# Kernel tuning notes

Measured on AMD Instinct MI355X. Metric: run time of the kernel, lower is better.

Reference implementation:

```python
import jax, jax.numpy as jnp
import numpy as np

B, S, D, H = 2, 2048, 1024, 16
Dh = D // H
ROPE_BASE = 10000.0


def _rope_cos_sin(seq_len, dh, dtype):
    inv_freq = 1.0 / (ROPE_BASE ** (jnp.arange(0, dh, 2, dtype=jnp.float32) / dh))
    t = jnp.arange(seq_len, dtype=jnp.float32)
    freqs = jnp.outer(t, inv_freq)              # (S, Dh/2)
    emb = jnp.concatenate([freqs, freqs], -1)   # (S, Dh)
    return jnp.cos(emb).astype(dtype), jnp.sin(emb).astype(dtype)


def _rotate_half(x):
    x1, x2 = jnp.split(x, 2, axis=-1)
    return jnp.concatenate([-x2, x1], axis=-1)


def setup_inputs() -> dict:
    key = jax.random.key(0)
    k1, k2, k3 = jax.random.split(key, 3)
    x = jax.random.normal(k1, (B, S, D), dtype=jnp.float32)
    w_qkv = jax.random.normal(k2, (D, 3 * D), dtype=jnp.float32) * (1.0 / np.sqrt(D))
    w_proj = jax.random.normal(k3, (D, D), dtype=jnp.float32) * (1.0 / np.sqrt(D))
    return {"x": x, "w_qkv": w_qkv, "w_proj": w_proj}


def reference(x, w_qkv, w_proj):
    b, s, d = x.shape
    qkv = x @ w_qkv                              # (B, S, 3D)
    q, k, v = jnp.split(qkv, 3, axis=-1)
    # (B, S, D) -> (B, H, S, Dh)
    shape_heads = lambda t: t.reshape(b, s, H, Dh).transpose(0, 2, 1, 3)
    q, k, v = shape_heads(q), shape_heads(k), shape_heads(v)
    cos, sin = _rope_cos_sin(s, Dh, x.dtype)     # (S, Dh) each
    cos = cos[None, None]                        # (1,1,S,Dh)
    sin = sin[None, None]
    q = q * cos + _rotate_half(q) * sin
    k = k * cos + _rotate_half(k) * sin
    attn = jnp.einsum('bhqd,bhkd->bhqk', q, k) / np.sqrt(Dh).astype(x.dtype)
    causal_mask = jnp.tril(jnp.ones((s, s), dtype=bool))
    attn = jnp.where(causal_mask, attn, -jnp.inf)
    attn = jax.nn.softmax(attn, axis=-1)
    out = jnp.einsum('bhqk,bhkd->bhqd', attn, v)
    out = out.transpose(0, 2, 1, 3).reshape(b, s, d)
    return out @ w_proj
```

## Files before the change

### kernel.cpp

```cpp
#include <hip/hip_runtime.h>


typedef unsigned short u16;
typedef __bf16 bf16x8 __attribute__((ext_vector_type(8)));
typedef unsigned short u16x8 __attribute__((ext_vector_type(8)));
typedef unsigned short u16x4 __attribute__((ext_vector_type(4)));
typedef float f32x4 __attribute__((ext_vector_type(4)));

#define B_ 2
#define S_ 2048
#define D_ 1024
#define H_ 16
#define DH_ 64
#define BS_ (B_ * S_)
#define N3_ (3 * D_)

__device__ __forceinline__ u16 f2bf(float f) {
  unsigned u = __float_as_uint(f);
  u += 0x7FFFu + ((u >> 16) & 1u);
  return (u16)(u >> 16);
}
__device__ __forceinline__ float bf2f(u16 s) {
  return __uint_as_float(((unsigned)s) << 16);
}

union BU { u16x8 u; bf16x8 b; };

__device__ __forceinline__ void store_c(u16* C, size_t i, float v) { C[i] = f2bf(v); }
__device__ __forceinline__ void store_c(float* C, size_t i, float v) { C[i] = v; }

#define SWZ(r) ((((r) >> 1) & 3) << 4)

__global__ __launch_bounds__(256) void k_cvt(const float* __restrict__ in,
                                             u16* __restrict__ out, int n4) {
  int i = blockIdx.x * 256 + threadIdx.x;
  if (i >= n4) return;
  const float4 f = ((const float4*)in)[i];
  u16x4 o;
  o[0] = f2bf(f.x); o[1] = f2bf(f.y); o[2] = f2bf(f.z); o[3] = f2bf(f.w);
  *(u16x4*)(out + (size_t)i * 4) = o;
}

__global__ __launch_bounds__(256) void k_cvt_T(const float* __restrict__ w,
                                               u16* __restrict__ wT, int R, int C) {
  __shared__ float tl[32][33];
  const int t = threadIdx.x;
  const int lrow = t >> 3, seg = t & 7;
  const int r0 = blockIdx.y * 32, c0 = blockIdx.x * 32;
  const float4 f = *(const float4*)(w + (size_t)(r0 + lrow) * C + c0 + seg * 4);
  tl[lrow][seg * 4 + 0] = f.x; tl[lrow][seg * 4 + 1] = f.y;
  tl[lrow][seg * 4 + 2] = f.z; tl[lrow][seg * 4 + 3] = f.w;
  __syncthreads();
  u16x4 o;
#pragma unroll
  for (int j = 0; j < 4; ++j) o[j] = f2bf(tl[seg * 4 + j][lrow]);
  *(u16x4*)(wT + (size_t)(c0 + lrow) * R + r0 + seg * 4) = o;
}

__global__ __launch_bounds__(256) void k_tab(float* __restrict__ ct, float* __restrict__ st) {
  const int idx = blockIdx.x * 256 + threadIdx.x;
  const int tpos = idx >> 5, i = idx & 31;
  const float invf = powf(10000.0f, -(float)i * (1.0f / 32.0f));
  const float a = (float)tpos * invf;
  ct[idx] = cosf(a);
  st[idx] = sinf(a);
}

template <typename OutT>
__global__ __launch_bounds__(256) void k_gemm(const u16* __restrict__ A,
                                              const u16* __restrict__ BT,
                                              OutT* __restrict__ C,
                                              int M, int N, int K) {
  __shared__ u16 la[128 * 32];
  __shared__ u16 lb[128 * 32];
  const int t = threadIdx.x;
  const int m0 = blockIdx.y * 128, n0 = blockIdx.x * 128;
  const int w = t >> 6, lane = t & 63;
  const int lr = lane & 15, lg = lane >> 4;
  const int wm = (w >> 1) * 64, wn = (w & 1) * 64;
  const int NK = K >> 5;

  const int r0s = t >> 2, i0 = t & 3;
  const int r1s = r0s + 64;

  f32x4 acc[4][4] = {};

  const u16* Ab = A + (size_t)m0 * K;
  const u16* Bb = BT + (size_t)n0 * K;

  u16x8 sa0 = *(const u16x8*)(Ab + (size_t)r0s * K + i0 * 8);
  u16x8 sa1 = *(const u16x8*)(Ab + (size_t)r1s * K + i0 * 8);
  u16x8 sb0 = *(const u16x8*)(Bb + (size_t)r0s * K + i0 * 8);
  u16x8 sb1 = *(const u16x8*)(Bb + (size_t)r1s * K + i0 * 8);
  u16x8 na0 = sa0, na1 = sa1, nb0 = sb0, nb1 = sb1;

  char* laq = (char*)la;
  char* lbq = (char*)lb;
  const int wo0 = r0s * 64 + ((i0 * 16) ^ SWZ(r0s));
  const int wo1 = r1s * 64 + ((i0 * 16) ^ SWZ(r1s));

  for (int kt = 0; kt < NK; ++kt) {
    __syncthreads();
    *(u16x8*)(laq + wo0) = sa0;
    *(u16x8*)(laq + wo1) = sa1;
    *(u16x8*)(lbq + wo0) = sb0;
    *(u16x8*)(lbq + wo1) = sb1;
    __syncthreads();
    if (kt + 1 < NK) {
      const u16* Ak = Ab + (size_t)(kt + 1) * 32;
      const u16* Bk = Bb + (size_t)(kt + 1) * 32;
      na0 = *(const u16x8*)(Ak + (size_t)r0s * K + i0 * 8);
      na1 = *(const u16x8*)(Ak + (size_t)r1s * K + i0 * 8);
      nb0 = *(const u16x8*)(Bk + (size_t)r0s * K + i0 * 8);
      nb1 = *(const u16x8*)(Bk + (size_t)r1s * K + i0 * 8);
    }
    BU af[4], bf_[4];
#pragma unroll
    for (int mi = 0; mi < 4; ++mi) {
      const int row = wm + mi * 16 + lr;
      af[mi].u = *(const u16x8*)(laq + row * 64 + ((lg * 16) ^ SWZ(row)));
      const int rowb = wn + mi * 16 + lr;
      bf_[mi].u = *(const u16x8*)(lbq + rowb * 64 + ((lg * 16) ^ SWZ(rowb)));
    }
#pragma unroll
    for (int mi = 0; mi < 4; ++mi)
#pragma unroll
      for (int ni = 0; ni < 4; ++ni)
        acc[mi][ni] = __builtin_amdgcn_mfma_f32_16x16x32_bf16(af[mi].b, bf_[ni].b,
                                                              acc[mi][ni], 0, 0, 0);
    sa0 = na0; sa1 = na1; sb0 = nb0; sb1 = nb1;
  }

#pragma unroll
  for (int mi = 0; mi < 4; ++mi)
#pragma unroll
    for (int ni = 0; ni < 4; ++ni)
#pragma unroll
      for (int r = 0; r < 4; ++r) {
        const int row = m0 + wm + mi * 16 + lg * 4 + r;
        const int col = n0 + wn + ni * 16 + lr;
        store_c(C, (size_t)row * N + col, acc[mi][ni][r]);
      }
}

__global__ __launch_bounds__(256) void k_prep(const u16* __restrict__ qkv,
                                              const float* __restrict__ ct,
                                              const float* __restrict__ st,
                                              u16* __restrict__ Q, u16* __restrict__ K,
                                              u16* __restrict__ Vt) {
  __shared__ u16 vl[64][72];
  const int stile = blockIdx.x, bh = blockIdx.y;
  const int b = bh >> 4, h = bh & 15;
  const int t = threadIdx.x;
  const int row = t >> 2, qr = t & 3;
  const int s = stile * 64 + row;
  const u16* base = qkv + (size_t)(b * S_ + s) * N3_ + h * DH_;
  const int d0 = qr * 8;
  float c[8], sn[8];
#pragma unroll
  for (int j = 0; j < 8; ++j) {
    c[j] = ct[s * 32 + d0 + j];
    sn[j] = st[s * 32 + d0 + j];
  }
#pragma unroll
  for (int part = 0; part < 2; ++part) {
    const u16* src = base + part * D_;
    u16x8 lo = *(const u16x8*)(src + d0);
    u16x8 hi = *(const u16x8*)(src + d0 + 32);
    u16x8 olo, ohi;
#pragma unroll
    for (int j = 0; j < 8; ++j) {
      float x1 = bf2f(lo[j]), x2 = bf2f(hi[j]);
      olo[j] = f2bf(x1 * c[j] - x2 * sn[j]);
      ohi[j] = f2bf(x2 * c[j] + x1 * sn[j]);
    }
    u16* dst = (part ? K : Q) + ((size_t)bh * S_ + s) * DH_;
    *(u16x8*)(dst + d0) = olo;
    *(u16x8*)(dst + d0 + 32) = ohi;
  }
  u16x8 v0 = *(const u16x8*)(base + 2 * D_ + qr * 16);
  u16x8 v1 = *(const u16x8*)(base + 2 * D_ + qr * 16 + 8);
#pragma unroll
  for (int j = 0; j < 8; ++j) {
    vl[qr * 16 + j][row] = v0[j];
    vl[qr * 16 + 8 + j][row] = v1[j];
  }
  __syncthreads();
  const int dh = row, sc = qr * 16;
  u16x8 o0, o1;
#pragma unroll
  for (int j = 0; j < 8; ++j) { o0[j] = vl[dh][sc + j]; o1[j] = vl[dh][sc + 8 + j]; }
  u16* vdst = Vt + ((size_t)bh * DH_ + dh) * S_ + stile * 64 + sc;
  *(u16x8*)vdst = o0;
  *(u16x8*)(vdst + 8) = o1;
}

__global__ __launch_bounds__(256, 4) void k_attn(const u16* __restrict__ Q,
                                                 const u16* __restrict__ K,
                                                 const u16* __restrict__ Vt,
                                                 u16* __restrict__ Ao) {
  __shared__ char kvb_[2][16384];
  __shared__ char plb[4][2048];
  const int bid = blockIdx.x;
  const int xcd = bid & 7, inner = bid >> 3;
  const int bh = xcd + 8 * (inner & 3);
  const int qt = 31 - (inner >> 2);
  const int t = threadIdx.x;
  const int w = t >> 6, lane = t & 63;
  const int lr = lane & 15, lg = lane >> 4;
  const int q0 = qt * 64 + w * 16;
  const int nt = qt + 1;

  const u16* Kbh = K + (size_t)bh * S_ * DH_;
  const u16* Vbh = Vt + (size_t)bh * DH_ * S_;

  const int srow = t >> 3;
  const int scol = (t & 7) * 8;

  const u16* Qb = Q + ((size_t)bh * S_ + q0) * DH_;
  BU qf0, qf1;
  qf0.u = *(const u16x8*)(Qb + lr * DH_ + lg * 8);
  qf1.u = *(const u16x8*)(Qb + lr * DH_ + 32 + lg * 8);

  f32x4 o[4] = {};
  float m = -1e30f, l = 0.f;
  char* plw = plb[w];
  const int psw = (lr & 7) << 4;

  u16x8 kreg[2], vreg[2];
#pragma unroll
  for (int c = 0; c < 2; ++c) {
    const int row = srow + 32 * c;
    kreg[c] = *(const u16x8*)(Kbh + (size_t)row * DH_ + scol);
    vreg[c] = *(const u16x8*)(Vbh + (size_t)row * S_ + scol);
  }
  {
    char* dst = kvb_[0];
#pragma unroll
    for (int c = 0; c < 2; ++c) {
      const int row = srow + 32 * c;
      const int off = row * 128 + ((scol * 2) ^ ((row & 7) << 4));
      *(u16x8*)(dst + off) = kreg[c];
      *(u16x8*)(dst + 8192 + off) = vreg[c];
    }
  }
  __syncthreads();

  int cur = 0;
  for (int it = 0; it < nt; ++it) {
    const int kv0 = it * 64;
    if (it + 1 < nt) {
      const int kvn = kv0 + 64;
#pragma unroll
      for (int c = 0; c < 2; ++c) {
        const int row = srow + 32 * c;
        kreg[c] = *(const u16x8*)(Kbh + (size_t)(kvn + row) * DH_ + scol);
        vreg[c] = *(const u16x8*)(Vbh + (size_t)row * S_ + kvn + scol);
      }
    }
    const char* base = kvb_[cur];
    f32x4 s[4] = {};
#pragma unroll
    for (int kvbi = 0; kvbi < 4; ++kvbi) {
      const int row = kvbi * 16 + lr;
      const int sw = (lr & 7) << 4;
      BU k0, k1;
      k0.u = *(const u16x8*)(base + row * 128 + ((lg * 16) ^ sw));
      k1.u = *(const u16x8*)(base + row * 128 + ((64 + lg * 16) ^ sw));
      s[kvbi] = __builtin_amdgcn_mfma_f32_16x16x32_bf16(k0.b, qf0.b, s[kvbi], 0, 0, 0);
      s[kvbi] = __builtin_amdgcn_mfma_f32_16x16x32_bf16(k1.b, qf1.b, s[kvbi], 0, 0, 0);
    }
    float p[16];
#pragma unroll
    for (int kvbi = 0; kvbi < 4; ++kvbi)
#pragma unroll
      for (int r = 0; r < 4; ++r) p[kvbi * 4 + r] = s[kvbi][r] * 0.125f;
    if (it == nt - 1) {
#pragma unroll
      for (int kvbi = 0; kvbi < 4; ++kvbi)
#pragma unroll
        for (int r = 0; r < 4; ++r)
          if (kv0 + kvbi * 16 + lg * 4 + r > q0 + lr) p[kvbi * 4 + r] = -1e30f;
    }
    float mx = p[0];
#pragma unroll
    for (int i = 1; i < 16; ++i) mx = fmaxf(mx, p[i]);
    mx = fmaxf(mx, __shfl_xor(mx, 16, 64));
    mx = fmaxf(mx, __shfl_xor(mx, 32, 64));
    const float mn = fmaxf(m, mx);
    const float al = __expf(m - mn);
    m = mn;
    float sm = 0.f;
#pragma unroll
    for (int i = 0; i < 16; ++i) { p[i] = __expf(p[i] - mn); sm += p[i]; }
    sm += __shfl_xor(sm, 16, 64);
    sm += __shfl_xor(sm, 32, 64);
    l = l * al + sm;
#pragma unroll
    for (int d = 0; d < 4; ++d)
#pragma unroll
      for (int r = 0; r < 4; ++r) o[d][r] *= al;
#pragma unroll
    for (int kvbi = 0; kvbi < 4; ++kvbi) {
      u16x4 w4;
#pragma unroll
      for (int r = 0; r < 4; ++r) w4[r] = f2bf(p[kvbi * 4 + r]);
      *(u16x4*)(plw + lr * 128 + ((kvbi * 32 + lg * 8) ^ psw)) = w4;
    }
    BU pf0, pf1;
    pf0.u = *(const u16x8*)(plw + lr * 128 + ((lg * 16) ^ psw));
    pf1.u = *(const u16x8*)(plw + lr * 128 + ((64 + lg * 16) ^ psw));
#pragma unroll
    for (int d = 0; d < 4; ++d) {
      const int row = d * 16 + lr;
      const int sw = (lr & 7) << 4;
      BU v0, v1;
      v0.u = *(const u16x8*)(base + 8192 + row * 128 + ((lg * 16) ^ sw));
      v1.u = *(const u16x8*)(base + 8192 + row * 128 + ((64 + lg * 16) ^ sw));
      o[d] = __builtin_amdgcn_mfma_f32_16x16x32_bf16(v0.b, pf0.b, o[d], 0, 0, 0);
      o[d] = __builtin_amdgcn_mfma_f32_16x16x32_bf16(v1.b, pf1.b, o[d], 0, 0, 0);
    }
    if (it + 1 < nt) {
      char* dst = kvb_[cur ^ 1];
#pragma unroll
      for (int c = 0; c < 2; ++c) {
        const int row = srow + 32 * c;
        const int off = row * 128 + ((scol * 2) ^ ((row & 7) << 4));
        *(u16x8*)(dst + off) = kreg[c];
        *(u16x8*)(dst + 8192 + off) = vreg[c];
      }
      __syncthreads();
    }
    cur ^= 1;
  }

  const float inv = 1.0f / l;
  const int b = bh >> 4, h = bh & 15;
  const size_t rowo = ((size_t)b * S_ + q0 + lr) * D_ + h * DH_;
#pragma unroll
  for (int d = 0; d < 4; ++d) {
    u16x4 w4;
#pragma unroll
    for (int r = 0; r < 4; ++r) w4[r] = f2bf(o[d][r] * inv);
    *(u16x4*)(Ao + rowo + d * 16 + lg * 4) = w4;
  }
}

extern "C" void kernel_launch(void* const* d_in, const int* in_sizes, int n_in,
                              void* d_out, int out_size, void* d_ws, size_t ws_size,
                              hipStream_t stream) {
  const float* x = (const float*)d_in[0];
  const float* wqkv = (const float*)d_in[1];
  const float* wproj = (const float*)d_in[2];
  float* out = (float*)d_out;
  char* ws = (char*)d_ws;

  u16* xb      = (u16*)(ws + 0);
  u16* wqkvT   = (u16*)(ws + 8388608);
  u16* wprojT  = (u16*)(ws + 14680064);
  u16* qkvb    = (u16*)(ws + 16777216);
  u16* Qb      = (u16*)(ws + 41943040);
  u16* Kb      = (u16*)(ws + 50331648);
  u16* Vtb     = (u16*)(ws + 58720256);
  u16* aob     = (u16*)(ws + 67108864);
  float* ct    = (float*)(ws + 75497472);
  float* stab  = (float*)(ws + 75759616);

  k_cvt<<<4096, 256, 0, stream>>>(x, xb, BS_ * D_ / 4);
  k_cvt_T<<<dim3(96, 32), 256, 0, stream>>>(wqkv, wqkvT, D_, N3_);
  k_cvt_T<<<dim3(32, 32), 256, 0, stream>>>(wproj, wprojT, D_, D_);
  k_tab<<<256, 256, 0, stream>>>(ct, stab);

  k_gemm<u16><<<dim3(24, 32), 256, 0, stream>>>(xb, wqkvT, qkvb, BS_, N3_, D_);
  k_prep<<<dim3(32, 32), 256, 0, stream>>>(qkvb, ct, stab, Qb, Kb, Vtb);
  k_attn<<<1024, 256, 0, stream>>>(Qb, Kb, Vtb, aob);
  k_gemm<float><<<dim3(8, 32), 256, 0, stream>>>(aob, wprojT, out, BS_, D_, D_);
}
```

Measured before the change: 126.5 us.

## Use direct global-to-LDS loads, pair causal q-tiles, fold softmax scale into Q

The GEMM now stages A/B tiles with global_load_lds into double-buffered LDS, dropping the register round trip and one barrier per k-step. Attention does the same for K/V, and each block handles a short and a long causal q-tile pair, halving the grid to balance work. The 1/sqrt(Dh) scale moves into the Q RoPE prep, and the softmax rescale is skipped unless the running max grows by more than 8. The launch bound drops to 2 blocks per CU. Risks: lower occupancy, the lazy-rescale threshold loosens overflow margins, and the LDS swizzle layout must match the reads exactly.

```diff
diff --git a/kernel.cpp b/kernel.cpp
--- a/kernel.cpp
+++ b/kernel.cpp
@@ -2,6 +2,7 @@
 
 
 typedef unsigned short u16;
+typedef unsigned int u32;
 typedef __bf16 bf16x8 __attribute__((ext_vector_type(8)));
 typedef unsigned short u16x8 __attribute__((ext_vector_type(8)));
 typedef unsigned short u16x4 __attribute__((ext_vector_type(4)));
@@ -29,7 +30,11 @@
 __device__ __forceinline__ void store_c(u16* C, size_t i, float v) { C[i] = f2bf(v); }
 __device__ __forceinline__ void store_c(float* C, size_t i, float v) { C[i] = v; }
 
-#define SWZ(r) ((((r) >> 1) & 3) << 4)
+__device__ __forceinline__ void gl16(const void* g, void* l) {
+  __builtin_amdgcn_global_load_lds(
+      (const __attribute__((address_space(1))) u32*)g,
+      (__attribute__((address_space(3))) u32*)l, 16, 0, 0);
+}
 
 __global__ __launch_bounds__(256) void k_cvt(const float* __restrict__ in,
                                              u16* __restrict__ out, int n4) {
@@ -71,8 +76,8 @@
                                               const u16* __restrict__ BT,
                                               OutT* __restrict__ C,
                                               int M, int N, int K) {
-  __shared__ u16 la[128 * 32];
-  __shared__ u16 lb[128 * 32];
+  __shared__ u16 la[2][128 * 32];
+  __shared__ u16 lb[2][128 * 32];
   const int t = threadIdx.x;
   const int m0 = blockIdx.y * 128, n0 = blockIdx.x * 128;
   const int w = t >> 6, lane = t & 63;
@@ -80,55 +85,50 @@
   const int wm = (w >> 1) * 64, wn = (w & 1) * 64;
   const int NK = K >> 5;
 
-  const int r0s = t >> 2, i0 = t & 3;
-  const int r1s = r0s + 64;
+  const int srow = lane >> 2;
+  const int sc = ((lane & 3) ^ ((lane >> 3) & 3)) * 8;
+  const u16* Ag = A + (size_t)(m0 + w * 32 + srow) * K + sc;
+  const u16* Bg = BT + (size_t)(n0 + w * 32 + srow) * K + sc;
+  const int ldsw = w * 1024;
 
   f32x4 acc[4][4] = {};
 
-  const u16* Ab = A + (size_t)m0 * K;
-  const u16* Bb = BT + (size_t)n0 * K;
-
-  u16x8 sa0 = *(const u16x8*)(Ab + (size_t)r0s * K + i0 * 8);
-  u16x8 sa1 = *(const u16x8*)(Ab + (size_t)r1s * K + i0 * 8);
-  u16x8 sb0 = *(const u16x8*)(Bb + (size_t)r0s * K + i0 * 8);
-  u16x8 sb1 = *(const u16x8*)(Bb + (size_t)r1s * K + i0 * 8);
-  u16x8 na0 = sa0, na1 = sa1, nb0 = sb0, nb1 = sb1;
-
-  char* laq = (char*)la;
-  char* lbq = (char*)lb;
-  const int wo0 = r0s * 64 + ((i0 * 16) ^ SWZ(r0s));
-  const int wo1 = r1s * 64 + ((i0 * 16) ^ SWZ(r1s));
-
+#pragma unroll
+  for (int i = 0; i < 2; ++i) {
+    gl16(Ag + (size_t)i * 16 * K, la[0] + ldsw + i * 512);
+    gl16(Bg + (size_t)i * 16 * K, lb[0] + ldsw + i * 512);
+  }
+  __syncthreads();
+
+  int cur = 0;
   for (int kt = 0; kt < NK; ++kt) {
+    if (kt + 1 < NK) {
+      const int ko = (kt + 1) * 32;
+#pragma unroll
+      for (int i = 0; i < 2; ++i) {
+        gl16(Ag + (size_t)i * 16 * K + ko, la[cur ^ 1] + ldsw + i * 512);
+        gl16(Bg + (size_t)i * 16 * K + ko, lb[cur ^ 1] + ldsw + i * 512);
+      }
+    }
+    const char* pa = (const char*)la[cur];
+    const char* pb = (const char*)lb[cur];
+    BU af[4], bfr[4];
+    const int rsw = ((lr >> 1) & 3);
+#pragma unroll
+    for (int mi = 0; mi < 4; ++mi) {
+      const int ra = wm + mi * 16 + lr;
+      af[mi].u = *(const u16x8*)(pa + ra * 64 + ((lg ^ rsw) * 16));
+      const int rb = wn + mi * 16 + lr;
+      bfr[mi].u = *(const u16x8*)(pb + rb * 64 + ((lg ^ rsw) * 16));
+    }
+#pragma unroll
+    for (int mi = 0; mi < 4; ++mi)
+#pragma unroll
+      for (int ni = 0; ni < 4; ++ni)
+        acc[mi][ni] = __builtin_amdgcn_mfma_f32_16x16x32_bf16(af[mi].b, bfr[ni].b,
+                                                              acc[mi][ni], 0, 0, 0);
     __syncthreads();
-    *(u16x8*)(laq + wo0) = sa0;
-    *(u16x8*)(laq + wo1) = sa1;
-    *(u16x8*)(lbq + wo0) = sb0;
-    *(u16x8*)(lbq + wo1) = sb1;
-    __syncthreads();
-    if (kt + 1 < NK) {
-      const u16* Ak = Ab + (size_t)(kt + 1) * 32;
-      const u16* Bk = Bb + (size_t)(kt + 1) * 32;
-      na0 = *(const u16x8*)(Ak + (size_t)r0s * K + i0 * 8);
-      na1 = *(const u16x8*)(Ak + (size_t)r1s * K + i0 * 8);
-      nb0 = *(const u16x8*)(Bk + (size_t)r0s * K + i0 * 8);
-      nb1 = *(const u16x8*)(Bk + (size_t)r1s * K + i0 * 8);
-    }
-    BU af[4], bf_[4];
-#pragma unroll
-    for (int mi = 0; mi < 4; ++mi) {
-      const int row = wm + mi * 16 + lr;
-      af[mi].u = *(const u16x8*)(laq + row * 64 + ((lg * 16) ^ SWZ(row)));
-      const int rowb = wn + mi * 16 + lr;
-      bf_[mi].u = *(const u16x8*)(lbq + rowb * 64 + ((lg * 16) ^ SWZ(rowb)));
-    }
-#pragma unroll
-    for (int mi = 0; mi < 4; ++mi)
-#pragma unroll
-      for (int ni = 0; ni < 4; ++ni)
-        acc[mi][ni] = __builtin_amdgcn_mfma_f32_16x16x32_bf16(af[mi].b, bf_[ni].b,
-                                                              acc[mi][ni], 0, 0, 0);
-    sa0 = na0; sa1 = na1; sb0 = nb0; sb1 = nb1;
+    cur ^= 1;
   }
 
 #pragma unroll
@@ -164,13 +164,14 @@
   }
 #pragma unroll
   for (int part = 0; part < 2; ++part) {
+    const float qs = (part == 0) ? 0.125f : 1.0f;
     const u16* src = base + part * D_;
     u16x8 lo = *(const u16x8*)(src + d0);
     u16x8 hi = *(const u16x8*)(src + d0 + 32);
     u16x8 olo, ohi;
 #pragma unroll
     for (int j = 0; j < 8; ++j) {
-      float x1 = bf2f(lo[j]), x2 = bf2f(hi[j]);
+      float x1 = bf2f(lo[j]) * qs, x2 = bf2f(hi[j]) * qs;
       olo[j] = f2bf(x1 * c[j] - x2 * sn[j]);
       ohi[j] = f2bf(x2 * c[j] + x1 * sn[j]);
     }
@@ -195,7 +196,7 @@
   *(u16x8*)(vdst + 8) = o1;
 }
 
-__global__ __launch_bounds__(256, 4) void k_attn(const u16* __restrict__ Q,
+__global__ __launch_bounds__(256, 2) void k_attn(const u16* __restrict__ Q,
                                                  const u16* __restrict__ K,
                                                  const u16* __restrict__ Vt,
                                                  u16* __restrict__ Ao) {
@@ -204,145 +205,135 @@
   const int bid = blockIdx.x;
   const int xcd = bid & 7, inner = bid >> 3;
   const int bh = xcd + 8 * (inner & 3);
-  const int qt = 31 - (inner >> 2);
+  const int f = inner >> 2;
   const int t = threadIdx.x;
   const int w = t >> 6, lane = t & 63;
   const int lr = lane & 15, lg = lane >> 4;
-  const int q0 = qt * 64 + w * 16;
-  const int nt = qt + 1;
 
   const u16* Kbh = K + (size_t)bh * S_ * DH_;
   const u16* Vbh = Vt + (size_t)bh * DH_ * S_;
 
-  const int srow = t >> 3;
-  const int scol = (t & 7) * 8;
-
-  const u16* Qb = Q + ((size_t)bh * S_ + q0) * DH_;
-  BU qf0, qf1;
-  qf0.u = *(const u16x8*)(Qb + lr * DH_ + lg * 8);
-  qf1.u = *(const u16x8*)(Qb + lr * DH_ + 32 + lg * 8);
-
-  f32x4 o[4] = {};
-  float m = -1e30f, l = 0.f;
+  const int sr = lane >> 3;
+  const int sc = ((lane & 7) ^ sr) * 8;
+  char* kd0 = kvb_[0] + w * 2048;
+  char* kd1 = kvb_[1] + w * 2048;
+
   char* plw = plb[w];
   const int psw = (lr & 7) << 4;
-
-  u16x8 kreg[2], vreg[2];
-#pragma unroll
-  for (int c = 0; c < 2; ++c) {
-    const int row = srow + 32 * c;
-    kreg[c] = *(const u16x8*)(Kbh + (size_t)row * DH_ + scol);
-    vreg[c] = *(const u16x8*)(Vbh + (size_t)row * S_ + scol);
-  }
-  {
-    char* dst = kvb_[0];
-#pragma unroll
-    for (int c = 0; c < 2; ++c) {
-      const int row = srow + 32 * c;
-      const int off = row * 128 + ((scol * 2) ^ ((row & 7) << 4));
-      *(u16x8*)(dst + off) = kreg[c];
-      *(u16x8*)(dst + 8192 + off) = vreg[c];
-    }
-  }
-  __syncthreads();
-
-  int cur = 0;
-  for (int it = 0; it < nt; ++it) {
-    const int kv0 = it * 64;
-    if (it + 1 < nt) {
-      const int kvn = kv0 + 64;
-#pragma unroll
-      for (int c = 0; c < 2; ++c) {
-        const int row = srow + 32 * c;
-        kreg[c] = *(const u16x8*)(Kbh + (size_t)(kvn + row) * DH_ + scol);
-        vreg[c] = *(const u16x8*)(Vbh + (size_t)row * S_ + kvn + scol);
-      }
-    }
-    const char* base = kvb_[cur];
-    f32x4 s[4] = {};
-#pragma unroll
-    for (int kvbi = 0; kvbi < 4; ++kvbi) {
-      const int row = kvbi * 16 + lr;
-      const int sw = (lr & 7) << 4;
-      BU k0, k1;
-      k0.u = *(const u16x8*)(base + row * 128 + ((lg * 16) ^ sw));
-      k1.u = *(const u16x8*)(base + row * 128 + ((64 + lg * 16) ^ sw));
-      s[kvbi] = __builtin_amdgcn_mfma_f32_16x16x32_bf16(k0.b, qf0.b, s[kvbi], 0, 0, 0);
-      s[kvbi] = __builtin_amdgcn_mfma_f32_16x16x32_bf16(k1.b, qf1.b, s[kvbi], 0, 0, 0);
-    }
-    float p[16];
-#pragma unroll
-    for (int kvbi = 0; kvbi < 4; ++kvbi)
-#pragma unroll
-      for (int r = 0; r < 4; ++r) p[kvbi * 4 + r] = s[kvbi][r] * 0.125f;
-    if (it == nt - 1) {
+  const int b = bh >> 4, h = bh & 15;
+
+  for (int ph = 0; ph < 2; ++ph) {
+    const int qt = ph ? 31 - f : f;
+    const int q0 = qt * 64 + w * 16;
+    const int nt = qt + 1;
+
+    const u16* Qb = Q + ((size_t)bh * S_ + q0) * DH_;
+    BU qf0, qf1;
+    qf0.u = *(const u16x8*)(Qb + lr * DH_ + lg * 8);
+    qf1.u = *(const u16x8*)(Qb + lr * DH_ + 32 + lg * 8);
+
+    f32x4 o[4] = {};
+    float m = -1e30f, l = 0.f;
+
+    __syncthreads();
+#pragma unroll
+    for (int j = 0; j < 2; ++j) {
+      const int row = w * 16 + j * 8 + sr;
+      gl16(Kbh + (size_t)row * DH_ + sc, kd0 + j * 1024);
+      gl16(Vbh + (size_t)row * S_ + sc, kd0 + 8192 + j * 1024);
+    }
+    __syncthreads();
+
+    int cur = 0;
+    for (int it = 0; it < nt; ++it) {
+      const int kv0 = it * 64;
+      if (it + 1 < nt) {
+        const int kvn = kv0 + 64;
+        char* nd = cur ? kd0 : kd1;
+#pragma unroll
+        for (int j = 0; j < 2; ++j) {
+          const int row = w * 16 + j * 8 + sr;
+          gl16(Kbh + (size_t)(kvn + row) * DH_ + sc, nd + j * 1024);
+          gl16(Vbh + (size_t)row * S_ + kvn + sc, nd + 8192 + j * 1024);
+        }
+      }
+      const char* base = kvb_[cur];
+      f32x4 s[4] = {};
+#pragma unroll
+      for (int kvbi = 0; kvbi < 4; ++kvbi) {
+        const int row = kvbi * 16 + lr;
+        const int sw = (lr & 7) << 4;
+        BU k0, k1;
+        k0.u = *(const u16x8*)(base + row * 128 + ((lg * 16) ^ sw));
+        k1.u = *(const u16x8*)(base + row * 128 + ((64 + lg * 16) ^ sw));
+        s[kvbi] = __builtin_amdgcn_mfma_f32_16x16x32_bf16(k0.b, qf0.b, s[kvbi], 0, 0, 0);
+        s[kvbi] = __builtin_amdgcn_mfma_f32_16x16x32_bf16(k1.b, qf1.b, s[kvbi], 0, 0, 0);
+      }
+      float p[16];
 #pragma unroll
       for (int kvbi = 0; kvbi < 4; ++kvbi)
 #pragma unroll
-        for (int r = 0; r < 4; ++r)
-          if (kv0 + kvbi * 16 + lg * 4 + r > q0 + lr) p[kvbi * 4 + r] = -1e30f;
-    }
-    float mx = p[0];
-#pragma unroll
-    for (int i = 1; i < 16; ++i) mx = fmaxf(mx, p[i]);
-    mx = fmaxf(mx, __shfl_xor(mx, 16, 64));
-    mx = fmaxf(mx, __shfl_xor(mx, 32, 64));
-    const float mn = fmaxf(m, mx);
-    const float al = __expf(m - mn);
-    m = mn;
-    float sm = 0.f;
-#pragma unroll
-    for (int i = 0; i < 16; ++i) { p[i] = __expf(p[i] - mn); sm += p[i]; }
-    sm += __shfl_xor(sm, 16, 64);
-    sm += __shfl_xor(sm, 32, 64);
-    l = l * al + sm;
-#pragma unroll
-    for (int d = 0; d < 4; ++d)
-#pragma unroll
-      for (int r = 0; r < 4; ++r) o[d][r] *= al;
-#pragma unroll
-    for (int kvbi = 0; kvbi < 4; ++kvbi) {
+        for (int r = 0; r < 4; ++r) p[kvbi * 4 + r] = s[kvbi][r];
+      if (it == nt - 1) {
+#pragma unroll
+        for (int kvbi = 0; kvbi < 4; ++kvbi)
+#pragma unroll
+          for (int r = 0; r < 4; ++r)
+            if (kv0 + kvbi * 16 + lg * 4 + r > q0 + lr) p[kvbi * 4 + r] = -1e30f;
+      }
+      float mx = p[0];
+#pragma unroll
+      for (int i = 1; i < 16; ++i) mx = fmaxf(mx, p[i]);
+      mx = fmaxf(mx, __shfl_xor(mx, 16, 64));
+      mx = fmaxf(mx, __shfl_xor(mx, 32, 64));
+      float al = 1.f;
+      const bool resc = (mx > m + 8.f);
+      if (resc) { al = __expf(m - mx); m = mx; }
+      float sm = 0.f;
+#pragma unroll
+      for (int i = 0; i < 16; ++i) { p[i] = __expf(p[i] - m); sm += p[i]; }
+      sm += __shfl_xor(sm, 16, 64);
+      sm += __shfl_xor(sm, 32, 64);
+      l = l * al + sm;
+      if (resc) {
+#pragma unroll
+        for (int d = 0; d < 4; ++d)
+#pragma unroll
+          for (int r = 0; r < 4; ++r) o[d][r] *= al;
+      }
+#pragma unroll
+      for (int kvbi = 0; kvbi < 4; ++kvbi) {
+        u16x4 w4;
+#pragma unroll
+        for (int r = 0; r < 4; ++r) w4[r] = f2bf(p[kvbi * 4 + r]);
+        *(u16x4*)(plw + lr * 128 + ((kvbi * 32 + lg * 8) ^ psw)) = w4;
+      }
+      BU pf0, pf1;
+      pf0.u = *(const u16x8*)(plw + lr * 128 + ((lg * 16) ^ psw));
+      pf1.u = *(const u16x8*)(plw + lr * 128 + ((64 + lg * 16) ^ psw));
+#pragma unroll
+      for (int d = 0; d < 4; ++d) {
+        const int row = d * 16 + lr;
+        const int sw = (lr & 7) << 4;
+        BU v0, v1;
+        v0.u = *(const u16x8*)(base + 8192 + row * 128 + ((lg * 16) ^ sw));
+        v1.u = *(const u16x8*)(base + 8192 + row * 128 + ((64 + lg * 16) ^ sw));
+        o[d] = __builtin_amdgcn_mfma_f32_16x16x32_bf16(v0.b, pf0.b, o[d], 0, 0, 0);
+        o[d] = __builtin_amdgcn_mfma_f32_16x16x32_bf16(v1.b, pf1.b, o[d], 0, 0, 0);
+      }
+      __syncthreads();
+      cur ^= 1;
+    }
+
+    const float inv = 1.0f / l;
+    const size_t rowo = ((size_t)b * S_ + q0 + lr) * D_ + h * DH_;
+#pragma unroll
+    for (int d = 0; d < 4; ++d) {
       u16x4 w4;
 #pragma unroll
-      for (int r = 0; r < 4; ++r) w4[r] = f2bf(p[kvbi * 4 + r]);
-      *(u16x4*)(plw + lr * 128 + ((kvbi * 32 + lg * 8) ^ psw)) = w4;
-    }
-    BU pf0, pf1;
-    pf0.u = *(const u16x8*)(plw + lr * 128 + ((lg * 16) ^ psw));
-    pf1.u = *(const u16x8*)(plw + lr * 128 + ((64 + lg * 16) ^ psw));
-#pragma unroll
-    for (int d = 0; d < 4; ++d) {
-      const int row = d * 16 + lr;
-      const int sw = (lr & 7) << 4;
-      BU v0, v1;
-      v0.u = *(const u16x8*)(base + 8192 + row * 128 + ((lg * 16) ^ sw));
-      v1.u = *(const u16x8*)(base + 8192 + row * 128 + ((64 + lg * 16) ^ sw));
-      o[d] = __builtin_amdgcn_mfma_f32_16x16x32_bf16(v0.b, pf0.b, o[d], 0, 0, 0);
-      o[d] = __builtin_amdgcn_mfma_f32_16x16x32_bf16(v1.b, pf1.b, o[d], 0, 0, 0);
-    }
-    if (it + 1 < nt) {
-      char* dst = kvb_[cur ^ 1];
-#pragma unroll
-      for (int c = 0; c < 2; ++c) {
-        const int row = srow + 32 * c;
-        const int off = row * 128 + ((scol * 2) ^ ((row & 7) << 4));
-        *(u16x8*)(dst + off) = kreg[c];
-        *(u16x8*)(dst + 8192 + off) = vreg[c];
-      }
-      __syncthreads();
-    }
-    cur ^= 1;
-  }
-
-  const float inv = 1.0f / l;
-  const int b = bh >> 4, h = bh & 15;
-  const size_t rowo = ((size_t)b * S_ + q0 + lr) * D_ + h * DH_;
-#pragma unroll
-  for (int d = 0; d < 4; ++d) {
-    u16x4 w4;
-#pragma unroll
-    for (int r = 0; r < 4; ++r) w4[r] = f2bf(o[d][r] * inv);
-    *(u16x4*)(Ao + rowo + d * 16 + lg * 4) = w4;
+      for (int r = 0; r < 4; ++r) w4[r] = f2bf(o[d][r] * inv);
+      *(u16x4*)(Ao + rowo + d * 16 + lg * 4) = w4;
+    }
   }
 }
 
@@ -373,6 +364,6 @@
 
   k_gemm<u16><<<dim3(24, 32), 256, 0, stream>>>(xb, wqkvT, qkvb, BS_, N3_, D_);
   k_prep<<<dim3(32, 32), 256, 0, stream>>>(qkvb, ct, stab, Qb, Kb, Vtb);
-  k_attn<<<1024, 256, 0, stream>>>(Qb, Kb, Vtb, aob);
+  k_attn<<<512, 256, 0, stream>>>(Qb, Kb, Vtb, aob);
   k_gemm<float><<<dim3(8, 32), 256, 0, stream>>>(aob, wprojT, out, BS_, D_, D_);
 }
```

After: 131.2 us. 1.04x slower.
